# Optimization experiments

Hardware: AMD Instinct MI355X
Metric: run time of the kernel (lower is better)

The kernel has to match this reference:

```python
import jax, jax.numpy as jnp
import numpy as np

C = 10.0
EMBEDDING_DIM = 128


def setup_inputs() -> dict:
    key = jax.random.key(0)
    k1, k2 = jax.random.split(key)
    B, P, D, N = 128, 128, 128, 4096
    mh_attn_out = jax.random.normal(k1, (B, P, D), dtype=jnp.float32)
    single_head_key = jax.random.normal(k2, (B, D, N), dtype=jnp.float32)
    mask = jnp.zeros((B, P, N), dtype=jnp.float32)  # additive mask (0 or -inf)
    return {"mh_attn_out": mh_attn_out, "single_head_key": single_head_key, "mask": mask}


def reference(mh_attn_out, single_head_key, mask):
    # score: [B, P, N]
    score = jnp.einsum('bpd,bdn->bpn', mh_attn_out, single_head_key)
    score_scaled = score / jnp.sqrt(jnp.float32(EMBEDDING_DIM))
    score_clipped = C * jnp.tanh(score_scaled)
    score_masked = score_clipped + mask
    probs = jax.nn.softmax(score_masked, axis=-1)
    return probs
```

## Files before the change

kernel.cpp:

```cpp
#include <hip/hip_runtime.h>
#include <math.h>

constexpr int BB = 128;
constexpr int PP = 128;
constexpr int DD = 128;
constexpr int NN = 4096;
constexpr float kC = 10.0f;
constexpr float k2InvSqrtD = 0.1767766952966369f;

constexpr int NTHR = 512;
constexpr int TEL = 272;

typedef float f32x4 __attribute__((ext_vector_type(4)));
typedef _Float16 f16x4 __attribute__((ext_vector_type(4)));
typedef _Float16 f16x8 __attribute__((ext_vector_type(8)));

__device__ __forceinline__ void st_nt_f4(float* p, float4 s) {
    f32x4 v = {s.x, s.y, s.z, s.w};
    __builtin_nontemporal_store(v, (f32x4*)p);
}

__device__ __forceinline__ f16x4 tr_read(unsigned addr) {
    f16x4 r;
    asm volatile("ds_read_b64_tr_b16 %0, %1" : "=v"(r) : "v"(addr));
    return r;
}

__device__ __forceinline__ float clip1(float s, float m) {
    const float e2 = __expf(s * k2InvSqrtD);
    const float r = __builtin_amdgcn_rcpf(e2 + 1.0f);
    return fmaf(-2.0f * kC, r, kC) + m;
}

__global__ __launch_bounds__(NTHR, 2)
void score_kernel(const float* __restrict__ A,
                  const float* __restrict__ K,
                  const float* __restrict__ M,
                  float* __restrict__ O,
                  float* __restrict__ ws) {
    __shared__ _Float16 Khi[64 * TEL];
    __shared__ _Float16 Klo[64 * TEL];

    const int l = blockIdx.x;
    const int b = l >> 5;
    const int ntb = l & 31;
    const int n_base = ntb * 128;

    const int tid = (int)threadIdx.x;
    const int lane = tid & 63;
    const int wid = tid >> 6;
    const int col = lane & 15;
    const int g = lane >> 4;
    const int kbase = 4 * g;

    const float* Kg = K + (size_t)b * DD * NN + n_base;
    {
        const int dl = tid >> 5;
        const int n4 = (tid & 31) * 4;
        const int tb = n4 >> 4;
        const int nin = n4 & 12;
        #pragma unroll
        for (int i = 0; i < 8; ++i) {
            const float4 v = *(const float4*)(Kg + (size_t)(16 * i + dl) * NN + n4);
            const float xs[4] = {v.x, v.y, v.z, v.w};
            f16x4 h, lo;
            #pragma unroll
            for (int e = 0; e < 4; ++e) {
                const _Float16 hh = (_Float16)xs[e];
                h[e] = hh;
                lo[e] = (_Float16)(xs[e] - (float)hh);
            }
            const int el = (i * 8 + tb) * TEL + dl * 16 + nin;
            *(f16x4*)&Khi[el] = h;
            *(f16x4*)&Klo[el] = lo;
        }
    }

    const float* Arow = A + (size_t)(b * PP + wid * 16 + col) * DD;
    f16x8 ah[4], al[4];
    #pragma unroll
    for (int kb = 0; kb < 4; ++kb) {
        #pragma unroll
        for (int j = 0; j < 8; ++j) {
            const int d = kb * 32 + kbase + (j & 3) + 16 * (j >> 2);
            const float x = Arow[d];
            const _Float16 h = (_Float16)x;
            ah[kb][j] = h;
            al[kb][j] = (_Float16)(x - (float)h);
        }
    }
    __syncthreads();

    const unsigned khi0 = (unsigned)(uintptr_t)&Khi[0] + (unsigned)lane * 8u;
    const unsigned klo0 = (unsigned)(uintptr_t)&Klo[0] + (unsigned)lane * 8u;

    const size_t mrow0 = (size_t)(b * PP + wid * 16 + kbase) * NN + n_base + col;

    float rsum[4] = {0.f, 0.f, 0.f, 0.f};
    float mv[4];
    #pragma unroll
    for (int j = 0; j < 4; ++j) mv[j] = M[mrow0 + (size_t)j * NN];

    #pragma unroll 2
    for (int nt = 0; nt < 8; ++nt) {
        float mvn[4] = {0.f, 0.f, 0.f, 0.f};
        if (nt < 7) {
            #pragma unroll
            for (int j = 0; j < 4; ++j)
                mvn[j] = M[mrow0 + (size_t)j * NN + (nt + 1) * 16];
        }

        f16x4 bh0[4], bh1[4], bl0[4], bl1[4];
        #pragma unroll
        for (int kb = 0; kb < 4; ++kb) {
            const unsigned t0 = (unsigned)(((2 * kb) * 8 + nt) * (TEL * 2));
            bh0[kb] = tr_read(khi0 + t0);
            bh1[kb] = tr_read(khi0 + t0 + 8u * (TEL * 2));
            bl0[kb] = tr_read(klo0 + t0);
            bl1[kb] = tr_read(klo0 + t0 + 8u * (TEL * 2));
        }
        asm volatile("s_waitcnt lgkmcnt(0)" ::: "memory");
        __builtin_amdgcn_sched_barrier(0);

        f32x4 acc = {0.f, 0.f, 0.f, 0.f};
        #pragma unroll
        for (int kb = 0; kb < 4; ++kb) {
            const f16x8 bh = __builtin_shufflevector(bh0[kb], bh1[kb], 0, 1, 2, 3, 4, 5, 6, 7);
            const f16x8 bl = __builtin_shufflevector(bl0[kb], bl1[kb], 0, 1, 2, 3, 4, 5, 6, 7);
            acc = __builtin_amdgcn_mfma_f32_16x16x32_f16(ah[kb], bh, acc, 0, 0, 0);
            acc = __builtin_amdgcn_mfma_f32_16x16x32_f16(ah[kb], bl, acc, 0, 0, 0);
            acc = __builtin_amdgcn_mfma_f32_16x16x32_f16(al[kb], bh, acc, 0, 0, 0);
        }

        #pragma unroll
        for (int j = 0; j < 4; ++j) {
            const size_t off = mrow0 + (size_t)j * NN + nt * 16;
            const float e = __expf(clip1(acc[j], mv[j]));
            O[off] = e;
            rsum[j] += e;
        }
        #pragma unroll
        for (int j = 0; j < 4; ++j) mv[j] = mvn[j];
    }

    #pragma unroll
    for (int j = 0; j < 4; ++j) {
        float s = rsum[j];
        s += __shfl_xor(s, 1);
        s += __shfl_xor(s, 2);
        s += __shfl_xor(s, 4);
        s += __shfl_xor(s, 8);
        rsum[j] = s;
    }
    if (col == 0) {
        #pragma unroll
        for (int j = 0; j < 4; ++j)
            ws[(size_t)(b * PP + wid * 16 + kbase + j) * 32 + ntb] = rsum[j];
    }
}

__global__ __launch_bounds__(256, 4)
void scale_kernel(float* __restrict__ O, const float* __restrict__ ws) {
    const int gtid = blockIdx.x * 256 + (int)threadIdx.x;
    const int row = gtid >> 5;
    const int seg = gtid & 31;

    const float* w = ws + (size_t)row * 32;
    float s = 0.f;
    #pragma unroll
    for (int i = 0; i < 8; ++i) {
        const float4 v = *(const float4*)(w + i * 4);
        s += (v.x + v.y) + (v.z + v.w);
    }
    const float inv = __builtin_amdgcn_rcpf(s);

    float4* R = (float4*)(O + (size_t)row * NN);
    #pragma unroll 8
    for (int i = 0; i < 32; ++i) {
        const int idx = i * 32 + seg;
        float4 v = R[idx];
        v.x *= inv; v.y *= inv; v.z *= inv; v.w *= inv;
        st_nt_f4((float*)&R[idx], v);
    }
}

extern "C" void kernel_launch(void* const* d_in, const int* in_sizes, int n_in,
                              void* d_out, int out_size, void* d_ws, size_t ws_size,
                              hipStream_t stream) {
    const float* A = (const float*)d_in[0];
    const float* K = (const float*)d_in[1];
    const float* M = (const float*)d_in[2];
    float* O = (float*)d_out;
    float* ws = (float*)d_ws;

    score_kernel<<<dim3(BB * 32), dim3(NTHR), 0, stream>>>(A, K, M, O, ws);
    scale_kernel<<<dim3(2048), dim3(256), 0, stream>>>(O, ws);
}
```

Baseline: 287.8 us.

## Halve K LDS staging into two column halves to double occupancy

Each block now stages the 128-column K tile as two 64-column halves in shared memory, using half the LDS, and the launch bound rises from 2 to 4 blocks per CU. Each half loads and converts its K slice, batches its mask loads, syncs, then runs the MFMA and softmax-exp loop over four 16-column tiles. The aim is more concurrent waves to hide global load and store latency. In exchange there is an extra barrier per block, a serial load-then-compute step within each block, and tighter register limits that may cause spills.

```diff
diff --git a/kernel.cpp b/kernel.cpp
--- a/kernel.cpp
+++ b/kernel.cpp
@@ -32,14 +32,14 @@
     return fmaf(-2.0f * kC, r, kC) + m;
 }
 
-__global__ __launch_bounds__(NTHR, 2)
+__global__ __launch_bounds__(NTHR, 4)
 void score_kernel(const float* __restrict__ A,
                   const float* __restrict__ K,
                   const float* __restrict__ M,
                   float* __restrict__ O,
                   float* __restrict__ ws) {
-    __shared__ _Float16 Khi[64 * TEL];
-    __shared__ _Float16 Klo[64 * TEL];
+    __shared__ _Float16 Khi[32 * TEL];
+    __shared__ _Float16 Klo[32 * TEL];
 
     const int l = blockIdx.x;
     const int b = l >> 5;
@@ -52,29 +52,6 @@
     const int col = lane & 15;
     const int g = lane >> 4;
     const int kbase = 4 * g;
-
-    const float* Kg = K + (size_t)b * DD * NN + n_base;
-    {
-        const int dl = tid >> 5;
-        const int n4 = (tid & 31) * 4;
-        const int tb = n4 >> 4;
-        const int nin = n4 & 12;
-        #pragma unroll
-        for (int i = 0; i < 8; ++i) {
-            const float4 v = *(const float4*)(Kg + (size_t)(16 * i + dl) * NN + n4);
-            const float xs[4] = {v.x, v.y, v.z, v.w};
-            f16x4 h, lo;
-            #pragma unroll
-            for (int e = 0; e < 4; ++e) {
-                const _Float16 hh = (_Float16)xs[e];
-                h[e] = hh;
-                lo[e] = (_Float16)(xs[e] - (float)hh);
-            }
-            const int el = (i * 8 + tb) * TEL + dl * 16 + nin;
-            *(f16x4*)&Khi[el] = h;
-            *(f16x4*)&Klo[el] = lo;
-        }
-    }
 
     const float* Arow = A + (size_t)(b * PP + wid * 16 + col) * DD;
     f16x8 ah[4], al[4];
@@ -89,58 +66,82 @@
             al[kb][j] = (_Float16)(x - (float)h);
         }
     }
-    __syncthreads();
 
+    const size_t mrow0 = (size_t)(b * PP + wid * 16 + kbase) * NN + n_base + col;
     const unsigned khi0 = (unsigned)(uintptr_t)&Khi[0] + (unsigned)lane * 8u;
     const unsigned klo0 = (unsigned)(uintptr_t)&Klo[0] + (unsigned)lane * 8u;
 
-    const size_t mrow0 = (size_t)(b * PP + wid * 16 + kbase) * NN + n_base + col;
+    const float* Kg = K + (size_t)b * DD * NN + n_base;
+    const int nl4 = (tid & 15) * 4;
+    const int d0 = tid >> 4;
+    const int ntile = nl4 >> 4;
+    const int nin = nl4 & 12;
 
     float rsum[4] = {0.f, 0.f, 0.f, 0.f};
-    float mv[4];
+
     #pragma unroll
-    for (int j = 0; j < 4; ++j) mv[j] = M[mrow0 + (size_t)j * NN];
+    for (int half = 0; half < 2; ++half) {
+        if (half) __syncthreads();
 
-    #pragma unroll 2
-    for (int nt = 0; nt < 8; ++nt) {
-        float mvn[4] = {0.f, 0.f, 0.f, 0.f};
-        if (nt < 7) {
+        #pragma unroll
+        for (int i = 0; i < 4; ++i) {
+            const int d = d0 + 32 * i;
+            const float4 v = *(const float4*)(Kg + (size_t)d * NN + half * 64 + nl4);
+            const float xs[4] = {v.x, v.y, v.z, v.w};
+            f16x4 h, lo;
+            #pragma unroll
+            for (int e = 0; e < 4; ++e) {
+                const _Float16 hh = (_Float16)xs[e];
+                h[e] = hh;
+                lo[e] = (_Float16)(xs[e] - (float)hh);
+            }
+            const int el = ((d >> 4) * 4 + ntile) * TEL + (d & 15) * 16 + nin;
+            *(f16x4*)&Khi[el] = h;
+            *(f16x4*)&Klo[el] = lo;
+        }
+
+        float mv[16];
+        #pragma unroll
+        for (int nt2 = 0; nt2 < 4; ++nt2)
             #pragma unroll
             for (int j = 0; j < 4; ++j)
-                mvn[j] = M[mrow0 + (size_t)j * NN + (nt + 1) * 16];
-        }
+                mv[nt2 * 4 + j] =
+                    M[mrow0 + (size_t)j * NN + half * 64 + nt2 * 16];
 
-        f16x4 bh0[4], bh1[4], bl0[4], bl1[4];
-        #pragma unroll
-        for (int kb = 0; kb < 4; ++kb) {
-            const unsigned t0 = (unsigned)(((2 * kb) * 8 + nt) * (TEL * 2));
-            bh0[kb] = tr_read(khi0 + t0);
-            bh1[kb] = tr_read(khi0 + t0 + 8u * (TEL * 2));
-            bl0[kb] = tr_read(klo0 + t0);
-            bl1[kb] = tr_read(klo0 + t0 + 8u * (TEL * 2));
-        }
-        asm volatile("s_waitcnt lgkmcnt(0)" ::: "memory");
-        __builtin_amdgcn_sched_barrier(0);
-
-        f32x4 acc = {0.f, 0.f, 0.f, 0.f};
-        #pragma unroll
-        for (int kb = 0; kb < 4; ++kb) {
-            const f16x8 bh = __builtin_shufflevector(bh0[kb], bh1[kb], 0, 1, 2, 3, 4, 5, 6, 7);
-            const f16x8 bl = __builtin_shufflevector(bl0[kb], bl1[kb], 0, 1, 2, 3, 4, 5, 6, 7);
-            acc = __builtin_amdgcn_mfma_f32_16x16x32_f16(ah[kb], bh, acc, 0, 0, 0);
-            acc = __builtin_amdgcn_mfma_f32_16x16x32_f16(ah[kb], bl, acc, 0, 0, 0);
-            acc = __builtin_amdgcn_mfma_f32_16x16x32_f16(al[kb], bh, acc, 0, 0, 0);
-        }
+        __syncthreads();
 
         #pragma unroll
-        for (int j = 0; j < 4; ++j) {
-            const size_t off = mrow0 + (size_t)j * NN + nt * 16;
-            const float e = __expf(clip1(acc[j], mv[j]));
-            O[off] = e;
-            rsum[j] += e;
+        for (int nt2 = 0; nt2 < 4; ++nt2) {
+            f16x4 bh0[4], bh1[4], bl0[4], bl1[4];
+            #pragma unroll
+            for (int kb = 0; kb < 4; ++kb) {
+                const unsigned t0 = (unsigned)(((2 * kb) * 4 + nt2) * 544);
+                bh0[kb] = tr_read(khi0 + t0);
+                bh1[kb] = tr_read(khi0 + t0 + 4u * 544u);
+                bl0[kb] = tr_read(klo0 + t0);
+                bl1[kb] = tr_read(klo0 + t0 + 4u * 544u);
+            }
+            asm volatile("s_waitcnt lgkmcnt(0)" ::: "memory");
+            __builtin_amdgcn_sched_barrier(0);
+
+            f32x4 acc = {0.f, 0.f, 0.f, 0.f};
+            #pragma unroll
+            for (int kb = 0; kb < 4; ++kb) {
+                const f16x8 bh = __builtin_shufflevector(bh0[kb], bh1[kb], 0, 1, 2, 3, 4, 5, 6, 7);
+                const f16x8 bl = __builtin_shufflevector(bl0[kb], bl1[kb], 0, 1, 2, 3, 4, 5, 6, 7);
+                acc = __builtin_amdgcn_mfma_f32_16x16x32_f16(ah[kb], bh, acc, 0, 0, 0);
+                acc = __builtin_amdgcn_mfma_f32_16x16x32_f16(ah[kb], bl, acc, 0, 0, 0);
+                acc = __builtin_amdgcn_mfma_f32_16x16x32_f16(al[kb], bh, acc, 0, 0, 0);
+            }
+
+            #pragma unroll
+            for (int j = 0; j < 4; ++j) {
+                const size_t off = mrow0 + (size_t)j * NN + half * 64 + nt2 * 16;
+                const float e = __expf(clip1(acc[j], mv[nt2 * 4 + j]));
+                O[off] = e;
+                rsum[j] += e;
+            }
         }
-        #pragma unroll
-        for (int j = 0; j < 4; ++j) mv[j] = mvn[j];
     }
 
     #pragma unroll
```

Measured after the change: 467.3 us. 62.3% more time.
